# Optimization experiments

Measured on AMD Instinct MI355X. Metric: run time of the kernel, lower is better.

## Reference

```python
import jax, jax.numpy as jnp
import numpy as np
from itertools import chain, combinations

OBS_DIM = 4096
LAT = 64
NG = 4
GS = OBS_DIM // NG  # 1024 features per group (round-robin i % NG == g)
B = 8192


def _powerset_mask(n):
    subsets = list(chain.from_iterable(combinations(range(n), r) for r in range(1, n + 1)))
    m = np.zeros((len(subsets), n), np.float32)
    for i, s in enumerate(subsets):
        m[i, list(s)] = 1.0
    return jnp.asarray(m)


SUBSET_MASK = _powerset_mask(NG)  # [S, G], S = 2^G - 1 = 15
GROUP_IDX = jnp.asarray(np.stack([np.arange(g, OBS_DIM, NG) for g in range(NG)]), dtype=jnp.int32)  # [G, GS]


def setup_inputs() -> dict:
    key = jax.random.key(0)
    ks = jax.random.split(key, 11)
    s = 0.05
    H = 2 * LAT  # encoder hidden / output width
    return {
        "X": jax.random.normal(ks[0], (B, OBS_DIM), jnp.float32),
        "eps": jax.random.normal(ks[1], (B, LAT), jnp.float32),
        "subset_idx": jax.random.randint(ks[2], (B,), 0, SUBSET_MASK.shape[0], dtype=jnp.int32),
        "enc_w1": jax.random.normal(ks[3], (NG, GS, H), jnp.float32) * s,
        "enc_b1": jnp.zeros((NG, H), jnp.float32),
        "enc_w2": jax.random.normal(ks[4], (NG, H, H), jnp.float32) * s,
        "enc_b2": jnp.zeros((NG, H), jnp.float32),
        "dec_w1": jax.random.normal(ks[5], (NG, LAT, LAT), jnp.float32) * s,
        "dec_b1": jnp.zeros((NG, LAT), jnp.float32),
        "dec_w2": jax.random.normal(ks[6], (NG, LAT, GS), jnp.float32) * s,
        "dec_b2": jnp.zeros((NG, GS), jnp.float32),
    }


def reference(X, eps, subset_idx, enc_w1, enc_b1, enc_w2, enc_b2, dec_w1, dec_b1, dec_w2, dec_b2):
    # ---- encode: per-group gather + tiny MLP (depth=2) ----
    Xg = X[:, GROUP_IDX]  # [B, G, GS] gather of group columns
    h = jax.nn.relu(jnp.einsum('bgi,gih->bgh', Xg, enc_w1) + enc_b1[None])  # [B, G, 2L]
    ml = jnp.einsum('bgh,gho->bgo', h, enc_w2) + enc_b2[None]               # [B, G, 2L]
    means, logvars = jnp.split(ml, 2, axis=-1)  # each [B, G, L]
    means = jnp.transpose(means, (0, 2, 1))     # [B, L, G] (tf stacks groups on axis=2)
    logvars = jnp.transpose(logvars, (0, 2, 1))

    # ---- mopoe: PoE over every non-empty subset of groups ----
    taus = jnp.exp(-logvars)                                   # [B, L, G]
    tau = jnp.einsum('blg,sg->bls', taus, SUBSET_MASK) + 1.0   # [B, L, S] (normalize_outp=True adds 1)
    m_means = jnp.einsum('blg,sg->bls', taus * means, SUBSET_MASK) / tau
    m_logvars = -jnp.log(tau)                                  # log(1/tau)

    # ---- reparameterize: pick one random subset per batch row ----
    sel = subset_idx[:, None, None].astype(jnp.int32)          # [B, 1, 1]
    smean = jnp.take_along_axis(m_means, sel, axis=-1)[..., 0]    # [B, L]
    slogv = jnp.take_along_axis(m_logvars, sel, axis=-1)[..., 0]  # [B, L]
    z = smean + eps * jnp.exp(0.5 * slogv)                     # [B, L]

    # ---- decode: per-group tiny MLP, scatter back to obs_dim ----
    hd = jax.nn.relu(jnp.einsum('bl,glm->bgm', z, dec_w1) + dec_b1[None])  # [B, G, L]
    outg = jnp.einsum('bgm,gmo->bgo', hd, dec_w2) + dec_b2[None]            # [B, G, GS]
    recon = jnp.zeros((X.shape[0], OBS_DIM), X.dtype).at[:, GROUP_IDX.reshape(-1)].set(
        outg.reshape(X.shape[0], -1))
    return recon
```

## Files before the change

### kernel.cpp

```cpp
#include <hip/hip_runtime.h>
#include <hip/hip_bf16.h>
#include <math.h>

#define B_TOT 8192
#define OBS   4096
#define NG    4
#define GSZ   1024
#define LATD  64
#define HDIM  128

typedef __attribute__((ext_vector_type(8))) short   short8_t;
typedef __attribute__((ext_vector_type(8))) unsigned short ushort8_t;
typedef __attribute__((ext_vector_type(4))) float   float4_t;

__constant__ int kMask[15] = {1,2,4,8, 3,5,9,6,10,12, 7,11,13,14, 15};

static __device__ __forceinline__ unsigned short f2b(float x) {
  __hip_bfloat16 b = __float2bfloat16(x);
  return *reinterpret_cast<unsigned short*>(&b);
}
static __device__ __forceinline__ unsigned int pack2(float lo, float hi) {
  return (unsigned int)f2b(lo) | ((unsigned int)f2b(hi) << 16);
}

#define N1 524288
#define N2 65536
#define N3 16384
#define N4 262144
__global__ __launch_bounds__(256) void k_prep(const float* __restrict__ w1,
                                              const float* __restrict__ w2,
                                              const float* __restrict__ w3,
                                              const float* __restrict__ w4,
                                              unsigned short* __restrict__ W1t,
                                              unsigned short* __restrict__ W2t,
                                              unsigned short* __restrict__ W3t,
                                              unsigned short* __restrict__ W4t) {
  const int i = blockIdx.x * 256 + threadIdx.x;
  if (i < N1) {
    const int g = i >> 17, rem = i & 131071;
    const int h = rem >> 10, k = rem & 1023;
    W1t[i] = f2b(w1[g * 131072 + k * 128 + h]);
  } else if (i < N1 + N2) {
    const int idx = i - N1;
    const int g = idx >> 14, rem = idx & 16383;
    const int o = rem >> 7, k = rem & 127;
    W2t[idx] = f2b(w2[g * 16384 + k * 128 + o]);
  } else if (i < N1 + N2 + N3) {
    const int idx = i - N1 - N2;
    const int g = idx >> 12, rem = idx & 4095;
    const int m = rem >> 6, k = rem & 63;
    W3t[idx] = f2b(w3[g * 4096 + k * 64 + m]);
  } else if (i < N1 + N2 + N3 + N4) {
    const int idx = i - N1 - N2 - N3;
    const int g = idx >> 16, rem = idx & 65535;
    const int o = rem >> 6, k = rem & 63;
    W4t[idx] = f2b(w4[g * 65536 + k * 1024 + o]);
  }
}

struct EncLds {
  union {
    unsigned short lsA[2][4][32][136];
    unsigned short hp[16][32][40];
    float mls[32][516];
  } u;
  unsigned short zb[32][72];
};
__global__ __launch_bounds__(512) void k_enc(const float* __restrict__ X,
                                             const unsigned short* __restrict__ W1t,
                                             const unsigned short* __restrict__ W2t,
                                             const unsigned short* __restrict__ W3t,
                                             const float* __restrict__ B1,
                                             const float* __restrict__ B2,
                                             const float* __restrict__ DB1,
                                             const float* __restrict__ eps,
                                             const int*   __restrict__ subset_idx,
                                             unsigned short* __restrict__ Hd) {
  __shared__ EncLds s;
  const int tid = threadIdx.x;
  const int w   = tid >> 6;
  const int l   = tid & 63;
  const int g   = w >> 1;
  const int hh  = (w & 1) * 64;
  const int rb  = blockIdx.x * 32;
  const int l15 = l & 15;
  const int oct = l >> 4;

  const int srow = tid >> 4;
  const int seg  = tid & 15;
  const float* xb = X + (size_t)(rb + srow) * OBS + seg * 32;

  float4_t q[8];
#pragma unroll
  for (int i = 0; i < 8; ++i) q[i] = *(const float4_t*)(xb + 4 * i);

  float4_t acc[2][4];
#pragma unroll
  for (int i = 0; i < 2; ++i)
#pragma unroll
    for (int j = 0; j < 4; ++j) acc[i][j] = (float4_t){0.f, 0.f, 0.f, 0.f};

#pragma unroll
  for (int gg = 0; gg < 4; ++gg) {
    uint4 val;
    val.x = pack2(q[0][gg], q[1][gg]);
    val.y = pack2(q[2][gg], q[3][gg]);
    val.z = pack2(q[4][gg], q[5][gg]);
    val.w = pack2(q[6][gg], q[7][gg]);
    *(uint4*)&s.u.lsA[0][gg][srow][seg * 8] = val;
  }
  __syncthreads();

  for (int c = 0; c < 8; ++c) {
    const int cur = c & 1;
    if (c < 7) {
#pragma unroll
      for (int i = 0; i < 8; ++i)
        q[i] = *(const float4_t*)(xb + (c + 1) * 512 + 4 * i);
    }

#pragma unroll
    for (int ks = 0; ks < 4; ++ks) {
      short8_t af[2], bf[4];
#pragma unroll
      for (int mi = 0; mi < 2; ++mi)
        af[mi] = *(const short8_t*)&s.u.lsA[cur][g][mi * 16 + l15][ks * 32 + oct * 8];
#pragma unroll
      for (int ni = 0; ni < 4; ++ni)
        bf[ni] = *(const short8_t*)(W1t +
                  (size_t)(g * 128 + hh + ni * 16 + l15) * GSZ +
                  c * 128 + ks * 32 + oct * 8);
#pragma unroll
      for (int mi = 0; mi < 2; ++mi)
#pragma unroll
        for (int ni = 0; ni < 4; ++ni)
          acc[mi][ni] = __builtin_amdgcn_mfma_f32_16x16x32_bf16(af[mi], bf[ni], acc[mi][ni], 0, 0, 0);
    }

    if (c < 7) {
#pragma unroll
      for (int gg = 0; gg < 4; ++gg) {
        uint4 val;
        val.x = pack2(q[0][gg], q[1][gg]);
        val.y = pack2(q[2][gg], q[3][gg]);
        val.z = pack2(q[4][gg], q[5][gg]);
        val.w = pack2(q[6][gg], q[7][gg]);
        *(uint4*)&s.u.lsA[cur ^ 1][gg][srow][seg * 8] = val;
      }
    }
    __syncthreads();
  }

#pragma unroll
  for (int ni = 0; ni < 4; ++ni) {
    const int cg    = hh + ni * 16 + l15;
    const int plane = (cg >> 5) * 4 + g;
    const int off   = cg & 31;
    const float b   = B1[g * 128 + cg];
#pragma unroll
    for (int mi = 0; mi < 2; ++mi) {
      const int row = mi * 16 + oct * 4;
#pragma unroll
      for (int j = 0; j < 4; ++j)
        s.u.hp[plane][row + j][off] = f2b(fmaxf(acc[mi][ni][j] + b, 0.0f));
    }
  }
  __syncthreads();

#pragma unroll
  for (int i = 0; i < 2; ++i)
#pragma unroll
    for (int j = 0; j < 4; ++j) acc[i][j] = (float4_t){0.f, 0.f, 0.f, 0.f};
  {
    const unsigned short* bbase = W2t + (size_t)(g * 128 + hh + l15) * HDIM + oct * 8;
#pragma unroll
    for (int ks = 0; ks < 4; ++ks) {
      short8_t af[2], bf[4];
#pragma unroll
      for (int mi = 0; mi < 2; ++mi)
        af[mi] = *(const short8_t*)(&s.u.hp[ks * 4 + g][mi * 16 + l15][oct * 8]);
#pragma unroll
      for (int ni = 0; ni < 4; ++ni)
        bf[ni] = *(const short8_t*)(bbase + (size_t)ni * 16 * HDIM + ks * 32);
#pragma unroll
      for (int mi = 0; mi < 2; ++mi)
#pragma unroll
        for (int ni = 0; ni < 4; ++ni)
          acc[mi][ni] = __builtin_amdgcn_mfma_f32_16x16x32_bf16(af[mi], bf[ni], acc[mi][ni], 0, 0, 0);
    }
  }
  __syncthreads();

#pragma unroll
  for (int ni = 0; ni < 4; ++ni) {
    const int col = g * 128 + hh + ni * 16 + l15;
    const float b = B2[col];
#pragma unroll
    for (int mi = 0; mi < 2; ++mi)
#pragma unroll
      for (int j = 0; j < 4; ++j)
        s.u.mls[mi * 16 + oct * 4 + j][col] = acc[mi][ni][j] + b;
  }
  __syncthreads();

#pragma unroll
  for (int qq = 0; qq < 4; ++qq) {
    const int idx = qq * 512 + tid;
    const int r   = idx >> 6;
    const int ll  = idx & 63;
    const int m   = kMask[subset_idx[rb + r]];
    float tau = 1.0f, num = 0.0f;
#pragma unroll
    for (int gg = 0; gg < 4; ++gg) {
      if (m & (1 << gg)) {
        const float lv = s.u.mls[r][gg * 128 + 64 + ll];
        const float mu = s.u.mls[r][gg * 128 + ll];
        const float t  = expf(-lv);
        tau += t;
        num = fmaf(t, mu, num);
      }
    }
    const float zv = num / tau + eps[(size_t)(rb + r) * LATD + ll] * rsqrtf(tau);
    s.zb[r][ll] = f2b(zv);
  }
  __syncthreads();

  const int mh = (w & 1) * 32;
  float4_t a3[2][2];
#pragma unroll
  for (int i = 0; i < 2; ++i)
#pragma unroll
    for (int j = 0; j < 2; ++j) a3[i][j] = (float4_t){0.f, 0.f, 0.f, 0.f};
  {
    const unsigned short* bbase = W3t + (size_t)(g * 64 + mh + l15) * LATD + oct * 8;
#pragma unroll
    for (int ks = 0; ks < 2; ++ks) {
      short8_t af[2], bf[2];
#pragma unroll
      for (int mi = 0; mi < 2; ++mi)
        af[mi] = *(const short8_t*)(&s.zb[mi * 16 + l15][ks * 32 + oct * 8]);
#pragma unroll
      for (int ni = 0; ni < 2; ++ni)
        bf[ni] = *(const short8_t*)(bbase + (size_t)ni * 16 * LATD + ks * 32);
#pragma unroll
      for (int mi = 0; mi < 2; ++mi)
#pragma unroll
        for (int ni = 0; ni < 2; ++ni)
          a3[mi][ni] = __builtin_amdgcn_mfma_f32_16x16x32_bf16(af[mi], bf[ni], a3[mi][ni], 0, 0, 0);
    }
  }
#pragma unroll
  for (int ni = 0; ni < 2; ++ni) {
    const int col = g * 64 + mh + ni * 16 + l15;
    const float b = DB1[col];
#pragma unroll
    for (int mi = 0; mi < 2; ++mi) {
      const int row = mi * 16 + oct * 4;
#pragma unroll
      for (int j = 0; j < 4; ++j)
        Hd[(size_t)(rb + row + j) * 256 + col] = f2b(fmaxf(a3[mi][ni][j] + b, 0.0f));
    }
  }
}

__global__ __launch_bounds__(512) void k_dec2(const unsigned short* __restrict__ Hd,
                                              const unsigned short* __restrict__ W4t,
                                              const float* __restrict__ Bb,
                                              float* __restrict__ Out) {
  __shared__ float obuf[32][264];

  const int tid = threadIdx.x;
  const int w   = tid >> 6;
  const int l   = tid & 63;
  const int g   = w >> 1;
  const int ohh = (w & 1) * 32;
  const int r0  = blockIdx.x * 32;
  const int ob  = blockIdx.y * 64;
  const int l15 = l & 15;
  const int oct = l >> 4;

  float4_t acc[2][2];
#pragma unroll
  for (int i = 0; i < 2; ++i)
#pragma unroll
    for (int j = 0; j < 2; ++j) acc[i][j] = (float4_t){0.f, 0.f, 0.f, 0.f};

#pragma unroll
  for (int ks = 0; ks < 2; ++ks) {
    short8_t af[2], bf[2];
#pragma unroll
    for (int mi = 0; mi < 2; ++mi)
      af[mi] = *(const short8_t*)(Hd + (size_t)(r0 + mi * 16 + l15) * 256 +
                                  g * 64 + ks * 32 + oct * 8);
#pragma unroll
    for (int ni = 0; ni < 2; ++ni)
      bf[ni] = *(const short8_t*)(W4t + (size_t)(g * 1024 + ob + ohh + ni * 16 + l15) * 64 +
                                  ks * 32 + oct * 8);
#pragma unroll
    for (int mi = 0; mi < 2; ++mi)
#pragma unroll
      for (int ni = 0; ni < 2; ++ni)
        acc[mi][ni] = __builtin_amdgcn_mfma_f32_16x16x32_bf16(af[mi], bf[ni], acc[mi][ni], 0, 0, 0);
  }

#pragma unroll
  for (int ni = 0; ni < 2; ++ni) {
    const int lo = ohh + ni * 16 + l15;
    const float b = Bb[g * 1024 + ob + lo];
#pragma unroll
    for (int mi = 0; mi < 2; ++mi) {
      const int rloc = mi * 16 + oct * 4;
#pragma unroll
      for (int j = 0; j < 4; ++j)
        obuf[rloc + j][4 * lo + g] = acc[mi][ni][j] + b;
    }
  }
  __syncthreads();

#pragma unroll
  for (int i = 0; i < 4; ++i) {
    const int q = tid + i * 512;
    const int row = q >> 6, c4 = q & 63;
    const float4 v = *(const float4*)&obuf[row][c4 * 4];
    *(float4*)(Out + (size_t)(r0 + row) * OBS + 4 * ob + c4 * 4) = v;
  }
}

extern "C" void kernel_launch(void* const* d_in, const int* in_sizes, int n_in,
                              void* d_out, int out_size, void* d_ws, size_t ws_size,
                              hipStream_t stream) {
  const float* X          = (const float*)d_in[0];
  const float* eps        = (const float*)d_in[1];
  const int*   subset_idx = (const int*)  d_in[2];
  const float* enc_w1     = (const float*)d_in[3];
  const float* enc_b1     = (const float*)d_in[4];
  const float* enc_w2     = (const float*)d_in[5];
  const float* enc_b2     = (const float*)d_in[6];
  const float* dec_w1     = (const float*)d_in[7];
  const float* dec_b1     = (const float*)d_in[8];
  const float* dec_w2     = (const float*)d_in[9];
  const float* dec_b2     = (const float*)d_in[10];
  float* out = (float*)d_out;

  char* wsb = (char*)d_ws;
  unsigned short* Hd  = (unsigned short*)wsb;
  unsigned short* W1t = (unsigned short*)(wsb + (4u << 20));
  unsigned short* W2t = (unsigned short*)(wsb + (5u << 20));
  unsigned short* W3t = (unsigned short*)(wsb + (5u << 20) + (128u << 10));
  unsigned short* W4t = (unsigned short*)(wsb + (5u << 20) + (160u << 10));

  k_prep<<<3392, 256, 0, stream>>>(enc_w1, enc_w2, dec_w1, dec_w2,
                                   W1t, W2t, W3t, W4t);
  k_enc<<<256, 512, 0, stream>>>(X, W1t, W2t, W3t, enc_b1, enc_b2, dec_b1,
                                 eps, subset_idx, Hd);
  k_dec2<<<dim3(256, 16), 512, 0, stream>>>(Hd, W4t, dec_b2, out);
}
```

Before: 121.4 us.

## Prepack weights in MFMA fragment order and halve encoder rows per block

```diff
diff --git a/kernel.cpp b/kernel.cpp
--- a/kernel.cpp
+++ b/kernel.cpp
@@ -8,6 +8,10 @@
 #define GSZ   1024
 #define LATD  64
 #define HDIM  128
+
+#define RS   136
+#define PLA  2184
+#define PSH  648
 
 typedef __attribute__((ext_vector_type(8))) short   short8_t;
 typedef __attribute__((ext_vector_type(8))) unsigned short ushort8_t;
@@ -31,180 +35,172 @@
                                               const float* __restrict__ w2,
                                               const float* __restrict__ w3,
                                               const float* __restrict__ w4,
-                                              unsigned short* __restrict__ W1t,
-                                              unsigned short* __restrict__ W2t,
-                                              unsigned short* __restrict__ W3t,
-                                              unsigned short* __restrict__ W4t) {
+                                              unsigned short* __restrict__ W1p,
+                                              unsigned short* __restrict__ W2p,
+                                              unsigned short* __restrict__ W3p,
+                                              unsigned short* __restrict__ W4p) {
   const int i = blockIdx.x * 256 + threadIdx.x;
   if (i < N1) {
-    const int g = i >> 17, rem = i & 131071;
-    const int h = rem >> 10, k = rem & 1023;
-    W1t[i] = f2b(w1[g * 131072 + k * 128 + h]);
+    const int j = i & 7, oct = (i >> 3) & 3, l15 = (i >> 5) & 15;
+    const int ni = (i >> 9) & 3, ks = (i >> 11) & 3, c = (i >> 13) & 7;
+    const int h2 = (i >> 16) & 1, g = (i >> 17) & 3;
+    const int k = c * 128 + (j & 3) * 32 + ks * 8 + oct * 2 + (j >> 2);
+    const int h = h2 * 64 + ni * 16 + l15;
+    W1p[i] = f2b(w1[g * 131072 + k * 128 + h]);
   } else if (i < N1 + N2) {
     const int idx = i - N1;
-    const int g = idx >> 14, rem = idx & 16383;
-    const int o = rem >> 7, k = rem & 127;
-    W2t[idx] = f2b(w2[g * 16384 + k * 128 + o]);
+    const int j = idx & 7, oct = (idx >> 3) & 3, l15 = (idx >> 5) & 15;
+    const int ni = (idx >> 9) & 3, ks = (idx >> 11) & 3;
+    const int h2 = (idx >> 13) & 1, g = (idx >> 14) & 3;
+    const int k = ks * 32 + oct * 8 + j;
+    const int h = h2 * 64 + ni * 16 + l15;
+    W2p[idx] = f2b(w2[g * 16384 + k * 128 + h]);
   } else if (i < N1 + N2 + N3) {
     const int idx = i - N1 - N2;
-    const int g = idx >> 12, rem = idx & 4095;
-    const int m = rem >> 6, k = rem & 63;
-    W3t[idx] = f2b(w3[g * 4096 + k * 64 + m]);
+    const int j = idx & 7, oct = (idx >> 3) & 3, l15 = (idx >> 5) & 15;
+    const int ni = (idx >> 9) & 1, ks = (idx >> 10) & 1;
+    const int h2 = (idx >> 11) & 1, g = (idx >> 12) & 3;
+    const int k = ks * 32 + oct * 8 + j;
+    const int m = h2 * 32 + ni * 16 + l15;
+    W3p[idx] = f2b(w3[g * 4096 + k * 64 + m]);
   } else if (i < N1 + N2 + N3 + N4) {
     const int idx = i - N1 - N2 - N3;
-    const int g = idx >> 16, rem = idx & 65535;
-    const int o = rem >> 6, k = rem & 63;
-    W4t[idx] = f2b(w4[g * 65536 + k * 1024 + o]);
+    const int j = idx & 7, oct = (idx >> 3) & 3, l15 = (idx >> 5) & 15;
+    const int ni = (idx >> 9) & 1, ks = (idx >> 10) & 1;
+    const int oh = (idx >> 11) & 1, ob = (idx >> 12) & 15, g = (idx >> 16) & 3;
+    const int k = ks * 32 + oct * 8 + j;
+    const int o = ob * 64 + oh * 32 + ni * 16 + l15;
+    W4p[idx] = f2b(w4[g * 65536 + k * 1024 + o]);
   }
 }
 
 struct EncLds {
   union {
-    unsigned short lsA[2][4][32][136];
-    unsigned short hp[16][32][40];
-    float mls[32][516];
+    unsigned short lA[2][4 * PLA];
+    unsigned short hp[16 * PSH];
+    float mls[16][516];
   } u;
-  unsigned short zb[32][72];
+  unsigned short zb[16][72];
 };
-__global__ __launch_bounds__(512) void k_enc(const float* __restrict__ X,
-                                             const unsigned short* __restrict__ W1t,
-                                             const unsigned short* __restrict__ W2t,
-                                             const unsigned short* __restrict__ W3t,
-                                             const float* __restrict__ B1,
-                                             const float* __restrict__ B2,
-                                             const float* __restrict__ DB1,
-                                             const float* __restrict__ eps,
-                                             const int*   __restrict__ subset_idx,
-                                             unsigned short* __restrict__ Hd) {
+__global__ __launch_bounds__(512, 4) void k_enc(const float* __restrict__ X,
+                                                const unsigned short* __restrict__ W1p,
+                                                const unsigned short* __restrict__ W2p,
+                                                const unsigned short* __restrict__ W3p,
+                                                const float* __restrict__ B1,
+                                                const float* __restrict__ B2,
+                                                const float* __restrict__ DB1,
+                                                const float* __restrict__ eps,
+                                                const int*   __restrict__ subset_idx,
+                                                unsigned short* __restrict__ Hd) {
   __shared__ EncLds s;
   const int tid = threadIdx.x;
   const int w   = tid >> 6;
   const int l   = tid & 63;
   const int g   = w >> 1;
-  const int hh  = (w & 1) * 64;
-  const int rb  = blockIdx.x * 32;
+  const int h2  = w & 1;
+  const int rb  = blockIdx.x * 16;
   const int l15 = l & 15;
   const int oct = l >> 4;
-
-  const int srow = tid >> 4;
-  const int seg  = tid & 15;
-  const float* xb = X + (size_t)(rb + srow) * OBS + seg * 32;
-
-  float4_t q[8];
-#pragma unroll
-  for (int i = 0; i < 8; ++i) q[i] = *(const float4_t*)(xb + 4 * i);
-
-  float4_t acc[2][4];
-#pragma unroll
-  for (int i = 0; i < 2; ++i)
-#pragma unroll
-    for (int j = 0; j < 4; ++j) acc[i][j] = (float4_t){0.f, 0.f, 0.f, 0.f};
-
-#pragma unroll
-  for (int gg = 0; gg < 4; ++gg) {
-    uint4 val;
-    val.x = pack2(q[0][gg], q[1][gg]);
-    val.y = pack2(q[2][gg], q[3][gg]);
-    val.z = pack2(q[4][gg], q[5][gg]);
-    val.w = pack2(q[6][gg], q[7][gg]);
-    *(uint4*)&s.u.lsA[0][gg][srow][seg * 8] = val;
-  }
-  __syncthreads();
+  const int lofs = (l15 * 4 + oct) * 8;
+
+  const int srow = tid >> 5;
+  const int seg  = tid & 31;
+  const float* xb = X + (size_t)(rb + srow) * OBS + seg * 4;
+
+  float4_t q0, q1, q2, q3;
+  q0 = *(const float4_t*)(xb + 0);
+  q1 = *(const float4_t*)(xb + 128);
+  q2 = *(const float4_t*)(xb + 256);
+  q3 = *(const float4_t*)(xb + 384);
+  {
+#pragma unroll
+    for (int gg = 0; gg < 4; ++gg) {
+      uint2 v;
+      v.x = pack2(q0[gg], q1[gg]);
+      v.y = pack2(q2[gg], q3[gg]);
+      *(uint2*)&s.u.lA[0][gg * PLA + srow * RS + seg * 4] = v;
+    }
+  }
+
+  float4_t acc[4];
+#pragma unroll
+  for (int j = 0; j < 4; ++j) acc[j] = (float4_t){0.f, 0.f, 0.f, 0.f};
+
+  const unsigned short* bb1 = W1p + (g * 2 + h2) * 65536 + lofs;
 
   for (int c = 0; c < 8; ++c) {
+    __syncthreads();
     const int cur = c & 1;
     if (c < 7) {
-#pragma unroll
-      for (int i = 0; i < 8; ++i)
-        q[i] = *(const float4_t*)(xb + (c + 1) * 512 + 4 * i);
-    }
-
+      const float* xn = xb + (c + 1) * 512;
+      q0 = *(const float4_t*)(xn + 0);
+      q1 = *(const float4_t*)(xn + 128);
+      q2 = *(const float4_t*)(xn + 256);
+      q3 = *(const float4_t*)(xn + 384);
+    }
 #pragma unroll
     for (int ks = 0; ks < 4; ++ks) {
-      short8_t af[2], bf[4];
-#pragma unroll
-      for (int mi = 0; mi < 2; ++mi)
-        af[mi] = *(const short8_t*)&s.u.lsA[cur][g][mi * 16 + l15][ks * 32 + oct * 8];
+      const short8_t af = *(const short8_t*)&s.u.lA[cur][g * PLA + l15 * RS + ks * 32 + oct * 8];
+      short8_t bf[4];
 #pragma unroll
       for (int ni = 0; ni < 4; ++ni)
-        bf[ni] = *(const short8_t*)(W1t +
-                  (size_t)(g * 128 + hh + ni * 16 + l15) * GSZ +
-                  c * 128 + ks * 32 + oct * 8);
-#pragma unroll
-      for (int mi = 0; mi < 2; ++mi)
-#pragma unroll
-        for (int ni = 0; ni < 4; ++ni)
-          acc[mi][ni] = __builtin_amdgcn_mfma_f32_16x16x32_bf16(af[mi], bf[ni], acc[mi][ni], 0, 0, 0);
-    }
-
+        bf[ni] = *(const short8_t*)(bb1 + c * 8192 + ks * 2048 + ni * 512);
+#pragma unroll
+      for (int ni = 0; ni < 4; ++ni)
+        acc[ni] = __builtin_amdgcn_mfma_f32_16x16x32_bf16(af, bf[ni], acc[ni], 0, 0, 0);
+    }
     if (c < 7) {
 #pragma unroll
       for (int gg = 0; gg < 4; ++gg) {
-        uint4 val;
-        val.x = pack2(q[0][gg], q[1][gg]);
-        val.y = pack2(q[2][gg], q[3][gg]);
-        val.z = pack2(q[4][gg], q[5][gg]);
-        val.w = pack2(q[6][gg], q[7][gg]);
-        *(uint4*)&s.u.lsA[cur ^ 1][gg][srow][seg * 8] = val;
+        uint2 v;
+        v.x = pack2(q0[gg], q1[gg]);
+        v.y = pack2(q2[gg], q3[gg]);
+        *(uint2*)&s.u.lA[cur ^ 1][gg * PLA + srow * RS + seg * 4] = v;
       }
     }
-    __syncthreads();
-  }
+  }
+  __syncthreads();
 
 #pragma unroll
   for (int ni = 0; ni < 4; ++ni) {
-    const int cg    = hh + ni * 16 + l15;
-    const int plane = (cg >> 5) * 4 + g;
-    const int off   = cg & 31;
-    const float b   = B1[g * 128 + cg];
-#pragma unroll
-    for (int mi = 0; mi < 2; ++mi) {
-      const int row = mi * 16 + oct * 4;
-#pragma unroll
-      for (int j = 0; j < 4; ++j)
-        s.u.hp[plane][row + j][off] = f2b(fmaxf(acc[mi][ni][j] + b, 0.0f));
-    }
-  }
-  __syncthreads();
-
-#pragma unroll
-  for (int i = 0; i < 2; ++i)
-#pragma unroll
-    for (int j = 0; j < 4; ++j) acc[i][j] = (float4_t){0.f, 0.f, 0.f, 0.f};
+    const int hcol = h2 * 64 + ni * 16 + l15;
+    const float b  = B1[g * 128 + hcol];
+    const int plane = (hcol >> 5) * 4 + g;
+    const int off   = hcol & 31;
+#pragma unroll
+    for (int j = 0; j < 4; ++j)
+      s.u.hp[plane * PSH + (oct * 4 + j) * 40 + off] = f2b(fmaxf(acc[ni][j] + b, 0.0f));
+  }
+  __syncthreads();
+
+#pragma unroll
+  for (int j = 0; j < 4; ++j) acc[j] = (float4_t){0.f, 0.f, 0.f, 0.f};
   {
-    const unsigned short* bbase = W2t + (size_t)(g * 128 + hh + l15) * HDIM + oct * 8;
+    const unsigned short* bb2 = W2p + (g * 2 + h2) * 8192 + lofs;
 #pragma unroll
     for (int ks = 0; ks < 4; ++ks) {
-      short8_t af[2], bf[4];
-#pragma unroll
-      for (int mi = 0; mi < 2; ++mi)
-        af[mi] = *(const short8_t*)(&s.u.hp[ks * 4 + g][mi * 16 + l15][oct * 8]);
-#pragma unroll
-      for (int ni = 0; ni < 4; ++ni)
-        bf[ni] = *(const short8_t*)(bbase + (size_t)ni * 16 * HDIM + ks * 32);
-#pragma unroll
-      for (int mi = 0; mi < 2; ++mi)
-#pragma unroll
-        for (int ni = 0; ni < 4; ++ni)
-          acc[mi][ni] = __builtin_amdgcn_mfma_f32_16x16x32_bf16(af[mi], bf[ni], acc[mi][ni], 0, 0, 0);
+      const short8_t af = *(const short8_t*)&s.u.hp[(ks * 4 + g) * PSH + l15 * 40 + oct * 8];
+#pragma unroll
+      for (int ni = 0; ni < 4; ++ni) {
+        const short8_t bf = *(const short8_t*)(bb2 + ks * 2048 + ni * 512);
+        acc[ni] = __builtin_amdgcn_mfma_f32_16x16x32_bf16(af, bf, acc[ni], 0, 0, 0);
+      }
     }
   }
   __syncthreads();
 
 #pragma unroll
   for (int ni = 0; ni < 4; ++ni) {
-    const int col = g * 128 + hh + ni * 16 + l15;
+    const int col = g * 128 + h2 * 64 + ni * 16 + l15;
     const float b = B2[col];
 #pragma unroll
-    for (int mi = 0; mi < 2; ++mi)
-#pragma unroll
-      for (int j = 0; j < 4; ++j)
-        s.u.mls[mi * 16 + oct * 4 + j][col] = acc[mi][ni][j] + b;
-  }
-  __syncthreads();
-
-#pragma unroll
-  for (int qq = 0; qq < 4; ++qq) {
+    for (int j = 0; j < 4; ++j)
+      s.u.mls[oct * 4 + j][col] = acc[ni][j] + b;
+  }
+  __syncthreads();
+
+#pragma unroll
+  for (int qq = 0; qq < 2; ++qq) {
     const int idx = qq * 512 + tid;
     const int r   = idx >> 6;
     const int ll  = idx & 63;
@@ -225,46 +221,33 @@
   }
   __syncthreads();
 
-  const int mh = (w & 1) * 32;
-  float4_t a3[2][2];
-#pragma unroll
-  for (int i = 0; i < 2; ++i)
-#pragma unroll
-    for (int j = 0; j < 2; ++j) a3[i][j] = (float4_t){0.f, 0.f, 0.f, 0.f};
+  float4_t a3[2];
+  a3[0] = (float4_t){0.f, 0.f, 0.f, 0.f};
+  a3[1] = (float4_t){0.f, 0.f, 0.f, 0.f};
   {
-    const unsigned short* bbase = W3t + (size_t)(g * 64 + mh + l15) * LATD + oct * 8;
+    const unsigned short* bb3 = W3p + (g * 2 + h2) * 2048 + lofs;
 #pragma unroll
     for (int ks = 0; ks < 2; ++ks) {
-      short8_t af[2], bf[2];
-#pragma unroll
-      for (int mi = 0; mi < 2; ++mi)
-        af[mi] = *(const short8_t*)(&s.zb[mi * 16 + l15][ks * 32 + oct * 8]);
-#pragma unroll
-      for (int ni = 0; ni < 2; ++ni)
-        bf[ni] = *(const short8_t*)(bbase + (size_t)ni * 16 * LATD + ks * 32);
-#pragma unroll
-      for (int mi = 0; mi < 2; ++mi)
-#pragma unroll
-        for (int ni = 0; ni < 2; ++ni)
-          a3[mi][ni] = __builtin_amdgcn_mfma_f32_16x16x32_bf16(af[mi], bf[ni], a3[mi][ni], 0, 0, 0);
+      const short8_t af = *(const short8_t*)&s.zb[l15][ks * 32 + oct * 8];
+#pragma unroll
+      for (int ni = 0; ni < 2; ++ni) {
+        const short8_t bf = *(const short8_t*)(bb3 + ks * 1024 + ni * 512);
+        a3[ni] = __builtin_amdgcn_mfma_f32_16x16x32_bf16(af, bf, a3[ni], 0, 0, 0);
+      }
     }
   }
 #pragma unroll
   for (int ni = 0; ni < 2; ++ni) {
-    const int col = g * 64 + mh + ni * 16 + l15;
+    const int col = g * 64 + h2 * 32 + ni * 16 + l15;
     const float b = DB1[col];
 #pragma unroll
-    for (int mi = 0; mi < 2; ++mi) {
-      const int row = mi * 16 + oct * 4;
-#pragma unroll
-      for (int j = 0; j < 4; ++j)
-        Hd[(size_t)(rb + row + j) * 256 + col] = f2b(fmaxf(a3[mi][ni][j] + b, 0.0f));
-    }
+    for (int j = 0; j < 4; ++j)
+      Hd[(size_t)(rb + oct * 4 + j) * 256 + col] = f2b(fmaxf(a3[ni][j] + b, 0.0f));
   }
 }
 
 __global__ __launch_bounds__(512) void k_dec2(const unsigned short* __restrict__ Hd,
-                                              const unsigned short* __restrict__ W4t,
+                                              const unsigned short* __restrict__ W4p,
                                               const float* __restrict__ Bb,
                                               float* __restrict__ Out) {
   __shared__ float obuf[32][264];
@@ -273,17 +256,20 @@
   const int w   = tid >> 6;
   const int l   = tid & 63;
   const int g   = w >> 1;
-  const int ohh = (w & 1) * 32;
+  const int oh  = w & 1;
   const int r0  = blockIdx.x * 32;
   const int ob  = blockIdx.y * 64;
   const int l15 = l & 15;
   const int oct = l >> 4;
+  const int lofs = (l15 * 4 + oct) * 8;
 
   float4_t acc[2][2];
 #pragma unroll
   for (int i = 0; i < 2; ++i)
 #pragma unroll
     for (int j = 0; j < 2; ++j) acc[i][j] = (float4_t){0.f, 0.f, 0.f, 0.f};
+
+  const unsigned short* bb4 = W4p + ((g * 16 + blockIdx.y) * 2 + oh) * 2048 + lofs;
 
 #pragma unroll
   for (int ks = 0; ks < 2; ++ks) {
@@ -294,8 +280,7 @@
                                   g * 64 + ks * 32 + oct * 8);
 #pragma unroll
     for (int ni = 0; ni < 2; ++ni)
-      bf[ni] = *(const short8_t*)(W4t + (size_t)(g * 1024 + ob + ohh + ni * 16 + l15) * 64 +
-                                  ks * 32 + oct * 8);
+      bf[ni] = *(const short8_t*)(bb4 + ks * 1024 + ni * 512);
 #pragma unroll
     for (int mi = 0; mi < 2; ++mi)
 #pragma unroll
@@ -305,7 +290,7 @@
 
 #pragma unroll
   for (int ni = 0; ni < 2; ++ni) {
-    const int lo = ohh + ni * 16 + l15;
+    const int lo = oh * 32 + ni * 16 + l15;
     const float b = Bb[g * 1024 + ob + lo];
 #pragma unroll
     for (int mi = 0; mi < 2; ++mi) {
@@ -344,14 +329,14 @@
 
   char* wsb = (char*)d_ws;
   unsigned short* Hd  = (unsigned short*)wsb;
-  unsigned short* W1t = (unsigned short*)(wsb + (4u << 20));
-  unsigned short* W2t = (unsigned short*)(wsb + (5u << 20));
-  unsigned short* W3t = (unsigned short*)(wsb + (5u << 20) + (128u << 10));
-  unsigned short* W4t = (unsigned short*)(wsb + (5u << 20) + (160u << 10));
+  unsigned short* W1p = (unsigned short*)(wsb + (4u << 20));
+  unsigned short* W2p = (unsigned short*)(wsb + (5u << 20));
+  unsigned short* W3p = (unsigned short*)(wsb + (5u << 20) + (128u << 10));
+  unsigned short* W4p = (unsigned short*)(wsb + (5u << 20) + (160u << 10));
 
   k_prep<<<3392, 256, 0, stream>>>(enc_w1, enc_w2, dec_w1, dec_w2,
-                                   W1t, W2t, W3t, W4t);
-  k_enc<<<256, 512, 0, stream>>>(X, W1t, W2t, W3t, enc_b1, enc_b2, dec_b1,
+                                   W1p, W2p, W3p, W4p);
+  k_enc<<<512, 512, 0, stream>>>(X, W1p, W2p, W3p, enc_b1, enc_b2, dec_b1,
                                  eps, subset_idx, Hd);
-  k_dec2<<<dim3(256, 16), 512, 0, stream>>>(Hd, W4t, dec_b2, out);
-}
+  k_dec2<<<dim3(256, 16), 512, 0, stream>>>(Hd, W4p, dec_b2, out);
+}
```

Measured after the change: 103.5 us. 1.17x faster.
